# Kernel tuning notes

Measured on AMD Instinct MI355X. Metric: run time of the kernel, lower is better.

## Reference

```python
import math
import jax, jax.numpy as jnp
import numpy as np

NH, NKV, HD, THETA = 32, 8, 128, 500000.0

def rotate_half(x):
    x1, x2 = jnp.split(x, 2, axis=-1)
    return jnp.concatenate((-x2, x1), axis=-1)

def rope_cos_sin(seq_len, dim, base, dtype):
    inv_freq = 1.0 / (base ** (jnp.arange(0, dim, 2, dtype=jnp.float32) / dim))
    t = jnp.arange(seq_len, dtype=jnp.float32)
    freqs = jnp.outer(t, inv_freq)              # [S, dim/2]
    emb = jnp.concatenate((freqs, freqs), -1)   # [S, dim]
    return jnp.cos(emb).astype(dtype), jnp.sin(emb).astype(dtype)

def setup_inputs() -> dict:
    key = jax.random.key(0)
    ks = jax.random.split(key, 5)
    B, S, H = 1, 2048, 4096
    sc = 1.0 / math.sqrt(H)
    return {
        'x':  jax.random.normal(ks[0], (B, S, H), jnp.float32),
        'wq': jax.random.normal(ks[1], (H, H), jnp.float32) * sc,
        'wk': jax.random.normal(ks[2], (NKV * HD, H), jnp.float32) * sc,
        'wv': jax.random.normal(ks[3], (NKV * HD, H), jnp.float32) * sc,
        'wo': jax.random.normal(ks[4], (H, H), jnp.float32) * sc,
    }

def attention(x, wq, wk, wv, wo):
    B, S, H = x.shape
    n_rep = NH // NKV
    q = (x @ wq.T).reshape(B, S, NH, HD).transpose(0, 2, 1, 3)    # [B,NH,S,HD]
    k = (x @ wk.T).reshape(B, S, NKV, HD).transpose(0, 2, 1, 3)   # [B,NKV,S,HD]
    v = (x @ wv.T).reshape(B, S, NKV, HD).transpose(0, 2, 1, 3)
    cos, sin = rope_cos_sin(S, HD, THETA, x.dtype)                # [S,HD]
    cos = cos[None, None]; sin = sin[None, None]
    q = q * cos + rotate_half(q) * sin
    k = k * cos + rotate_half(k) * sin
    k = jnp.repeat(k, n_rep, axis=1)                               # [B,NH,S,HD]
    v = jnp.repeat(v, n_rep, axis=1)
    scores = jnp.einsum('bhqd,bhkd->bhqk', q, k) / math.sqrt(HD)
    causal = jnp.tril(jnp.ones((S, S), dtype=bool))
    scores = jnp.where(causal, scores, jnp.finfo(scores.dtype).min)
    probs = jax.nn.softmax(scores, axis=-1)
    out = jnp.einsum('bhqk,bhkd->bhqd', probs, v)                  # [B,NH,S,HD]
    out = out.transpose(0, 2, 1, 3).reshape(B, S, H)
    return out @ wo.T

def reference(x, wq, wk, wv, wo):
    return attention(x, wq, wk, wv, wo)
```

## Files before the change

### kernel.cpp

```cpp
#include <hip/hip_runtime.h>
#include <hip/hip_bf16.h>
#include <math.h>

typedef __bf16 bf16x8 __attribute__((ext_vector_type(8)));
typedef __bf16 bf16x4 __attribute__((ext_vector_type(4)));
typedef unsigned short u16x8 __attribute__((ext_vector_type(8)));
typedef float  f32x4  __attribute__((ext_vector_type(4)));

constexpr int kS   = 2048;
constexpr int kH   = 4096;
constexpr int kNH  = 32;
constexpr int kNKV = 8;
constexpr int kHD  = 128;
constexpr int kQKV = kH + 2 * kNKV * kHD;
constexpr int kKOff = kH;
constexpr int kVOff = kH + kNKV * kHD;

__global__ void cast_bf16(const float* __restrict__ in, __bf16* __restrict__ out, int n4) {
    int i = blockIdx.x * blockDim.x + threadIdx.x;
    if (i < n4) {
        float4 f = ((const float4*)in)[i];
        bf16x4 o;
        o[0] = (__bf16)f.x; o[1] = (__bf16)f.y; o[2] = (__bf16)f.z; o[3] = (__bf16)f.w;
        ((bf16x4*)out)[i] = o;
    }
}

__global__ void cast_all(const float* __restrict__ x, const float* __restrict__ wq,
                         const float* __restrict__ wk, const float* __restrict__ wv,
                         __bf16* __restrict__ xb, __bf16* __restrict__ wqkv) {
    int i = blockIdx.x * 256 + threadIdx.x;
    float4 f;
    __bf16* dst;
    int di;
    if (i < (1 << 21)) {
        f = ((const float4*)x)[i];
        dst = xb; di = i;
    } else {
        int j = i - (1 << 21);
        const float4* s = (j < (1 << 22)) ? ((const float4*)wq + j)
                        : (j < (5 << 20)) ? ((const float4*)wk + (j - (1 << 22)))
                                          : ((const float4*)wv + (j - (5 << 20)));
        f = *s;
        dst = wqkv; di = j;
    }
    bf16x4 o;
    o[0] = (__bf16)f.x; o[1] = (__bf16)f.y; o[2] = (__bf16)f.z; o[3] = (__bf16)f.w;
    ((bf16x4*)dst)[di] = o;
}

constexpr int BM = 128, BN = 128, BK = 64;

__device__ inline void gld16(const __bf16* g, __bf16* l) {
    __builtin_amdgcn_global_load_lds((const __attribute__((address_space(1))) void*)g,
                                     (__attribute__((address_space(3))) void*)l, 16, 0, 0);
}

template <typename OutT>
__global__ __launch_bounds__(256) void gemm_nt(const __bf16* __restrict__ A,
                                               const __bf16* __restrict__ B,
                                               OutT* __restrict__ C,
                                               int M, int N, int K) {
    __shared__ __align__(16) __bf16 As[BM * BK];
    __shared__ __align__(16) __bf16 Bs[BN * BK];
    const int tid  = threadIdx.x;
    const int w    = tid >> 6, lane = tid & 63;
    const int m0   = blockIdx.y * BM, n0 = blockIdx.x * BN;
    const int wm   = (w >> 1) * 64, wn = (w & 1) * 64;
    const int lr   = lane & 15, g8 = lane >> 4;

    const int l3 = lane >> 3;
    const int lc = (lane & 7) ^ l3;
    const __bf16 *gA[4], *gB[4];
    __bf16 *lA[4], *lB[4];
#pragma unroll
    for (int c = 0; c < 4; c++) {
        int G = w * 4 + c;
        gA[c] = A + (size_t)(m0 + G * 8 + l3) * K + lc * 8;
        gB[c] = B + (size_t)(n0 + G * 8 + l3) * K + lc * 8;
        lA[c] = As + G * 512;
        lB[c] = Bs + G * 512;
    }

    f32x4 acc[4][4];
#pragma unroll
    for (int i = 0; i < 4; i++)
#pragma unroll
        for (int j = 0; j < 4; j++) acc[i][j] = (f32x4)(0.f);

    for (int k0 = 0; k0 < K; k0 += BK) {
#pragma unroll
        for (int c = 0; c < 4; c++) {
            gld16(gA[c] + k0, lA[c]);
            gld16(gB[c] + k0, lB[c]);
        }
        __syncthreads();

        const int rx = lr & 7;
#pragma unroll
        for (int kc = 0; kc < 2; kc++) {
            bf16x8 af[4], bfr[4];
#pragma unroll
            for (int i = 0; i < 4; i++)
                af[i]  = *(const bf16x8*)&As[(wm + i * 16 + lr) * BK + (((kc * 4 + g8) ^ rx) * 8)];
#pragma unroll
            for (int j = 0; j < 4; j++)
                bfr[j] = *(const bf16x8*)&Bs[(wn + j * 16 + lr) * BK + (((kc * 4 + g8) ^ rx) * 8)];
#pragma unroll
            for (int i = 0; i < 4; i++)
#pragma unroll
                for (int j = 0; j < 4; j++)
                    acc[i][j] = __builtin_amdgcn_mfma_f32_16x16x32_bf16(af[i], bfr[j], acc[i][j], 0, 0, 0);
        }
        __syncthreads();
    }

    const int cr = g8 * 4, cc = lr;
#pragma unroll
    for (int i = 0; i < 4; i++)
#pragma unroll
        for (int j = 0; j < 4; j++) {
            OutT* Cp = C + (size_t)(m0 + wm + i * 16 + cr) * N + (n0 + wn + j * 16 + cc);
#pragma unroll
            for (int r = 0; r < 4; r++) Cp[(size_t)r * N] = (OutT)acc[i][j][r];
        }
}

__global__ void rope_qkv(__bf16* __restrict__ qkv) {
    int idx  = blockIdx.x * 256 + threadIdx.x;
    int d    = idx & 63;
    int rest = idx >> 6;
    int hh   = rest % (kNH + kNKV);
    int s    = rest / (kNH + kNKV);
    float inv_freq = powf(500000.0f, -(float)d * (1.0f / 64.0f));
    float sn, cs;
    sincosf((float)s * inv_freq, &sn, &cs);
    __bf16* base = qkv + (size_t)s * kQKV + ((hh < kNH) ? hh * kHD : kKOff + (hh - kNH) * kHD);
    float sc = (hh < kNH) ? 0.088388347648318447f : 1.0f;
    float a = (float)base[d], b = (float)base[d + 64];
    base[d]      = (__bf16)((a * cs - b * sn) * sc);
    base[d + 64] = (__bf16)((b * cs + a * sn) * sc);
}

constexpr int VTP = 72;

__global__ __launch_bounds__(256) void flash_attn(const __bf16* __restrict__ qkv,
                                                  __bf16* __restrict__ ob) {
    __shared__ __align__(16) __bf16 Ks[64 * 128];
    __shared__ __align__(16) __bf16 Vt[128 * VTP];
    __shared__ __align__(16) __bf16 Ps[4 * 16 * 64];

    const int tid  = threadIdx.x;
    const int wave = tid >> 6, lane = tid & 63;
    const int bx   = blockIdx.x;
    const int kvh  = bx & 7;
    const int qt   = 127 - (bx >> 3);
    const int h    = kvh * 4 + wave;
    const int r    = lane & 15, g = lane >> 4;
    const int r7   = r & 7;
    const int qglob = qt * 16 + r;

    __bf16* Pw = Ps + wave * 16 * 64;
    const __bf16* kbase = qkv + kKOff + kvh * kHD;
    const __bf16* vbase = qkv + kVOff + kvh * kHD;

    int krow[4], kgc[4];
#pragma unroll
    for (int c = 0; c < 4; c++) {
        krow[c] = wave * 16 + c * 4 + (lane >> 4);
        kgc[c]  = (lane & 15) ^ (krow[c] & 15);
    }

    bf16x8 qfrag[4];
    const __bf16* qrow = qkv + (size_t)(qt * 16 + r) * kQKV + h * kHD + g * 8;
#pragma unroll
    for (int c = 0; c < 4; c++) qfrag[c] = *(const bf16x8*)(qrow + c * 32);

    f32x4 o[8];
#pragma unroll
    for (int dt = 0; dt < 8; dt++) o[dt] = (f32x4)(0.f);
    float mrow = -3.0e38f, lrow = 0.f;

    const int nkt = qt / 4 + 1;
    for (int kt = 0; kt < nkt; ++kt) {
#pragma unroll
        for (int c = 0; c < 4; c++)
            gld16(kbase + (size_t)(kt * 64 + krow[c]) * kQKV + kgc[c] * 8,
                  Ks + (wave * 4 + c) * 512);
#pragma unroll
        for (int i = 0; i < 2; i++) {
            int task = i * 256 + tid;
            int p = task & 31, c = task >> 5;
            const __bf16* v0 = vbase + (size_t)(kt * 64 + 2 * p) * kQKV + c * 8;
            u16x8 a = __builtin_bit_cast(u16x8, *(const bf16x8*)v0);
            u16x8 b = __builtin_bit_cast(u16x8, *(const bf16x8*)(v0 + kQKV));
#pragma unroll
            for (int j = 0; j < 8; j++) {
                unsigned int pk = (unsigned int)a[j] | ((unsigned int)b[j] << 16);
                *(unsigned int*)(Vt + (c * 8 + j) * VTP + 2 * p) = pk;
            }
        }
        __syncthreads();

        f32x4 st[4];
#pragma unroll
        for (int t = 0; t < 4; t++) st[t] = (f32x4)(0.f);
#pragma unroll
        for (int c = 0; c < 4; c++) {
#pragma unroll
            for (int t = 0; t < 4; t++) {
                bf16x8 kf = *(const bf16x8*)&Ks[(t * 16 + r) * 128 + (((c * 4 + g) ^ r) * 8)];
                st[t] = __builtin_amdgcn_mfma_f32_16x16x32_bf16(kf, qfrag[c], st[t], 0, 0, 0);
            }
        }

        if (kt == nkt - 1) {
#pragma unroll
            for (int t = 0; t < 4; t++)
#pragma unroll
                for (int reg = 0; reg < 4; reg++) {
                    int key = kt * 64 + t * 16 + g * 4 + reg;
                    if (key > qglob) st[t][reg] = -3.0e38f;
                }
        }

        float mloc = -3.0e38f;
#pragma unroll
        for (int t = 0; t < 4; t++)
#pragma unroll
            for (int reg = 0; reg < 4; reg++) mloc = fmaxf(mloc, st[t][reg]);
        mloc = fmaxf(mloc, __shfl_xor(mloc, 16));
        mloc = fmaxf(mloc, __shfl_xor(mloc, 32));
        float mnew  = fmaxf(mrow, mloc);
        float alpha = __expf(mrow - mnew);
        mrow = mnew;
        float lsum = 0.f;
#pragma unroll
        for (int t = 0; t < 4; t++)
#pragma unroll
            for (int reg = 0; reg < 4; reg++) {
                float pv = __expf(st[t][reg] - mnew);
                st[t][reg] = pv;
                lsum += pv;
            }
        lsum += __shfl_xor(lsum, 16);
        lsum += __shfl_xor(lsum, 32);
        lrow = lrow * alpha + lsum;

        float ar[4];
#pragma unroll
        for (int reg = 0; reg < 4; reg++) ar[reg] = __shfl(alpha, g * 4 + reg);
#pragma unroll
        for (int dt = 0; dt < 8; dt++)
#pragma unroll
            for (int reg = 0; reg < 4; reg++) o[dt][reg] *= ar[reg];

#pragma unroll
        for (int t = 0; t < 4; t++) {
            bf16x4 pb;
#pragma unroll
            for (int j = 0; j < 4; j++) pb[j] = (__bf16)st[t][j];
            int p8 = t * 4 + g;
            *(bf16x4*)&Pw[r * 64 + (((p8 >> 1) ^ r7) * 8) + ((p8 & 1) * 4)] = pb;
        }
        __asm__ volatile("s_waitcnt lgkmcnt(0)" ::: "memory");

#pragma unroll
        for (int kc = 0; kc < 2; kc++) {
            bf16x8 pf = *(const bf16x8*)&Pw[r * 64 + (((kc * 4 + g) ^ r7) * 8)];
#pragma unroll
            for (int dt = 0; dt < 8; dt++) {
                bf16x8 vf = *(const bf16x8*)&Vt[(dt * 16 + r) * VTP + kc * 32 + g * 8];
                o[dt] = __builtin_amdgcn_mfma_f32_16x16x32_bf16(pf, vf, o[dt], 0, 0, 0);
            }
        }
        __syncthreads();
    }

    float linv = 1.f / lrow;
    float lr4[4];
#pragma unroll
    for (int reg = 0; reg < 4; reg++) lr4[reg] = __shfl(linv, g * 4 + reg);
#pragma unroll
    for (int dt = 0; dt < 8; dt++)
#pragma unroll
        for (int reg = 0; reg < 4; reg++) {
            int qq = g * 4 + reg, dd = dt * 16 + r;
            ob[(size_t)(qt * 16 + qq) * kH + h * kHD + dd] = (__bf16)(o[dt][reg] * lr4[reg]);
        }
}

extern "C" void kernel_launch(void* const* d_in, const int* in_sizes, int n_in,
                              void* d_out, int out_size, void* d_ws, size_t ws_size,
                              hipStream_t stream) {
    const float* x  = (const float*)d_in[0];
    const float* wq = (const float*)d_in[1];
    const float* wk = (const float*)d_in[2];
    const float* wv = (const float*)d_in[3];
    const float* wo = (const float*)d_in[4];
    float* out = (float*)d_out;

    char* p = (char*)d_ws;
    auto alloc = [&](size_t bytes) {
        char* r = p;
        p += (bytes + 255) & ~(size_t)255;
        return r;
    };
    __bf16* xb    = (__bf16*)alloc((size_t)kS * kH * 2);
    __bf16* wqkvb = (__bf16*)alloc((size_t)kQKV * kH * 2);
    __bf16* qkv   = (__bf16*)alloc((size_t)kS * kQKV * 2);
    __bf16* ao    = xb;
    __bf16* wob   = wqkvb;

    cast_all<<<dim3(1 << 15), 256, 0, stream>>>(x, wq, wk, wv, xb, wqkvb);

    gemm_nt<__bf16><<<dim3(kQKV / BN, kS / BM), 256, 0, stream>>>(xb, wqkvb, qkv, kS, kQKV, kH);

    rope_qkv<<<dim3(kS * (kNH + kNKV) * 64 / 256), 256, 0, stream>>>(qkv);

    cast_bf16<<<dim3((kH * kH / 4) / 256), 256, 0, stream>>>(wo, wob, kH * kH / 4);

    flash_attn<<<dim3(kNKV * (kS / 16)), 256, 0, stream>>>(qkv, ao);

    gemm_nt<float><<<dim3(kH / BN, kS / BM), 256, 0, stream>>>(ao, wob, out, kS, kH, kH);
}
```

Measured before the change: 528.1 us.

## Fuse RoPE into QKV GEMM epilogue and register-prefetch K/V in flash attention

```diff
diff --git a/kernel.cpp b/kernel.cpp
--- a/kernel.cpp
+++ b/kernel.cpp
@@ -56,7 +56,7 @@
                                      (__attribute__((address_space(3))) void*)l, 16, 0, 0);
 }
 
-template <typename OutT>
+template <typename OutT, bool ROPE>
 __global__ __launch_bounds__(256) void gemm_nt(const __bf16* __restrict__ A,
                                                const __bf16* __restrict__ B,
                                                OutT* __restrict__ C,
@@ -66,8 +66,13 @@
     const int tid  = threadIdx.x;
     const int w    = tid >> 6, lane = tid & 63;
     const int m0   = blockIdx.y * BM, n0 = blockIdx.x * BN;
-    const int wm   = (w >> 1) * 64, wn = (w & 1) * 64;
+    const int wm   = (w >> 1) * 64;
+    const int wn2  = (w & 1);
     const int lr   = lane & 15, g8 = lane >> 4;
+
+    int jt[4];
+#pragma unroll
+    for (int j = 0; j < 4; j++) jt[j] = wn2 * 2 + (j & 1) + ((j >> 1) << 2);
 
     const int l3 = lane >> 3;
     const int lc = (lane & 7) ^ l3;
@@ -105,7 +110,7 @@
                 af[i]  = *(const bf16x8*)&As[(wm + i * 16 + lr) * BK + (((kc * 4 + g8) ^ rx) * 8)];
 #pragma unroll
             for (int j = 0; j < 4; j++)
-                bfr[j] = *(const bf16x8*)&Bs[(wn + j * 16 + lr) * BK + (((kc * 4 + g8) ^ rx) * 8)];
+                bfr[j] = *(const bf16x8*)&Bs[(jt[j] * 16 + lr) * BK + (((kc * 4 + g8) ^ rx) * 8)];
 #pragma unroll
             for (int i = 0; i < 4; i++)
 #pragma unroll
@@ -116,36 +121,43 @@
     }
 
     const int cr = g8 * 4, cc = lr;
+
+    if (ROPE && n0 < kVOff) {
+        const float qs = (n0 < kKOff) ? 0.088388347648318447f : 1.0f;
+        float invf[2];
+#pragma unroll
+        for (int p = 0; p < 2; p++)
+            invf[p] = powf(500000.0f, -(float)(wn2 * 32 + p * 16 + cc) * (1.0f / 64.0f));
+#pragma unroll
+        for (int i = 0; i < 4; i++)
+#pragma unroll
+            for (int reg = 0; reg < 4; reg++) {
+                float s = (float)(m0 + wm + i * 16 + cr + reg);
+#pragma unroll
+                for (int p = 0; p < 2; p++) {
+                    float sn, cs;
+                    sincosf(s * invf[p], &sn, &cs);
+                    float a = acc[i][p][reg], b = acc[i][p + 2][reg];
+                    acc[i][p][reg]     = (a * cs - b * sn) * qs;
+                    acc[i][p + 2][reg] = (b * cs + a * sn) * qs;
+                }
+            }
+    }
+
 #pragma unroll
     for (int i = 0; i < 4; i++)
 #pragma unroll
         for (int j = 0; j < 4; j++) {
-            OutT* Cp = C + (size_t)(m0 + wm + i * 16 + cr) * N + (n0 + wn + j * 16 + cc);
+            OutT* Cp = C + (size_t)(m0 + wm + i * 16 + cr) * N + (n0 + jt[j] * 16 + cc);
 #pragma unroll
             for (int r = 0; r < 4; r++) Cp[(size_t)r * N] = (OutT)acc[i][j][r];
         }
 }
 
-__global__ void rope_qkv(__bf16* __restrict__ qkv) {
-    int idx  = blockIdx.x * 256 + threadIdx.x;
-    int d    = idx & 63;
-    int rest = idx >> 6;
-    int hh   = rest % (kNH + kNKV);
-    int s    = rest / (kNH + kNKV);
-    float inv_freq = powf(500000.0f, -(float)d * (1.0f / 64.0f));
-    float sn, cs;
-    sincosf((float)s * inv_freq, &sn, &cs);
-    __bf16* base = qkv + (size_t)s * kQKV + ((hh < kNH) ? hh * kHD : kKOff + (hh - kNH) * kHD);
-    float sc = (hh < kNH) ? 0.088388347648318447f : 1.0f;
-    float a = (float)base[d], b = (float)base[d + 64];
-    base[d]      = (__bf16)((a * cs - b * sn) * sc);
-    base[d + 64] = (__bf16)((b * cs + a * sn) * sc);
-}
-
 constexpr int VTP = 72;
 
-__global__ __launch_bounds__(256) void flash_attn(const __bf16* __restrict__ qkv,
-                                                  __bf16* __restrict__ ob) {
+__global__ __launch_bounds__(256, 3) void flash_attn(const __bf16* __restrict__ qkv,
+                                                     __bf16* __restrict__ ob) {
     __shared__ __align__(16) __bf16 Ks[64 * 128];
     __shared__ __align__(16) __bf16 Vt[128 * VTP];
     __shared__ __align__(16) __bf16 Ps[4 * 16 * 64];
@@ -164,11 +176,14 @@
     const __bf16* kbase = qkv + kKOff + kvh * kHD;
     const __bf16* vbase = qkv + kVOff + kvh * kHD;
 
-    int krow[4], kgc[4];
-#pragma unroll
-    for (int c = 0; c < 4; c++) {
-        krow[c] = wave * 16 + c * 4 + (lane >> 4);
-        kgc[c]  = (lane & 15) ^ (krow[c] & 15);
+    const int kr   = tid >> 4;
+    const int kc16 = tid & 15;
+    int vp[2], vc[2];
+#pragma unroll
+    for (int i = 0; i < 2; i++) {
+        int task = i * 256 + tid;
+        vp[i] = task & 31;
+        vc[i] = task >> 5;
     }
 
     bf16x8 qfrag[4];
@@ -182,25 +197,39 @@
     float mrow = -3.0e38f, lrow = 0.f;
 
     const int nkt = qt / 4 + 1;
+
+    bf16x8 kreg[4];
+    bf16x8 vreg[2][2];
+    auto issue = [&](int kt) {
+#pragma unroll
+        for (int c = 0; c < 4; c++)
+            kreg[c] = *(const bf16x8*)(kbase + (size_t)(kt * 64 + kr + c * 16) * kQKV + kc16 * 8);
+#pragma unroll
+        for (int i = 0; i < 2; i++) {
+            const __bf16* v0 = vbase + (size_t)(kt * 64 + 2 * vp[i]) * kQKV + vc[i] * 8;
+            vreg[i][0] = *(const bf16x8*)v0;
+            vreg[i][1] = *(const bf16x8*)(v0 + kQKV);
+        }
+    };
+
+    issue(0);
     for (int kt = 0; kt < nkt; ++kt) {
+        if (kt) __syncthreads();
 #pragma unroll
         for (int c = 0; c < 4; c++)
-            gld16(kbase + (size_t)(kt * 64 + krow[c]) * kQKV + kgc[c] * 8,
-                  Ks + (wave * 4 + c) * 512);
+            *(bf16x8*)&Ks[(kr + c * 16) * 128 + ((kc16 ^ kr) * 8)] = kreg[c];
 #pragma unroll
         for (int i = 0; i < 2; i++) {
-            int task = i * 256 + tid;
-            int p = task & 31, c = task >> 5;
-            const __bf16* v0 = vbase + (size_t)(kt * 64 + 2 * p) * kQKV + c * 8;
-            u16x8 a = __builtin_bit_cast(u16x8, *(const bf16x8*)v0);
-            u16x8 b = __builtin_bit_cast(u16x8, *(const bf16x8*)(v0 + kQKV));
+            u16x8 a = __builtin_bit_cast(u16x8, vreg[i][0]);
+            u16x8 b = __builtin_bit_cast(u16x8, vreg[i][1]);
 #pragma unroll
             for (int j = 0; j < 8; j++) {
                 unsigned int pk = (unsigned int)a[j] | ((unsigned int)b[j] << 16);
-                *(unsigned int*)(Vt + (c * 8 + j) * VTP + 2 * p) = pk;
+                *(unsigned int*)(Vt + (vc[i] * 8 + j) * VTP + 2 * vp[i]) = pk;
             }
         }
         __syncthreads();
+        if (kt + 1 < nkt) issue(kt + 1);
 
         f32x4 st[4];
 #pragma unroll
@@ -274,7 +303,6 @@
                 o[dt] = __builtin_amdgcn_mfma_f32_16x16x32_bf16(pf, vf, o[dt], 0, 0, 0);
             }
         }
-        __syncthreads();
     }
 
     float linv = 1.f / lrow;
@@ -314,13 +342,11 @@
 
     cast_all<<<dim3(1 << 15), 256, 0, stream>>>(x, wq, wk, wv, xb, wqkvb);
 
-    gemm_nt<__bf16><<<dim3(kQKV / BN, kS / BM), 256, 0, stream>>>(xb, wqkvb, qkv, kS, kQKV, kH);
-
-    rope_qkv<<<dim3(kS * (kNH + kNKV) * 64 / 256), 256, 0, stream>>>(qkv);
+    gemm_nt<__bf16, true><<<dim3(kQKV / BN, kS / BM), 256, 0, stream>>>(xb, wqkvb, qkv, kS, kQKV, kH);
 
     cast_bf16<<<dim3((kH * kH / 4) / 256), 256, 0, stream>>>(wo, wob, kH * kH / 4);
 
     flash_attn<<<dim3(kNKV * (kS / 16)), 256, 0, stream>>>(qkv, ao);
 
-    gemm_nt<float><<<dim3(kH / BN, kS / BM), 256, 0, stream>>>(ao, wob, out, kS, kH, kH);
-}
+    gemm_nt<float, false><<<dim3(kH / BN, kS / BM), 256, 0, stream>>>(ao, wob, out, kS, kH, kH);
+}
```

After: 580.0 us. 1.1x slower.
